# Optimization experiments

Measured on AMD Instinct MI355X. Metric: run time of the kernel, lower is better.

Reference implementation:

```python
import jax, jax.numpy as jnp
import numpy as np

N_ELEMENTS = 64  # StructureElementLayer(n_elements=64)


def setup_inputs() -> dict:
    key = jax.random.key(0)
    k1, k2 = jax.random.split(key)
    # x: [N, C, T, V] skeleton sequence (batch, coord channels, time, joints)
    x = jax.random.normal(k1, (256, 3, 256, 25), dtype=jnp.float32)
    # StructureElementLayer parameters (torch.rand init / ones*3 init)
    centres = jax.random.uniform(k2, (N_ELEMENTS, 2), dtype=jnp.float32)
    sharpness = jnp.ones((N_ELEMENTS, 2), dtype=jnp.float32) * 3.0
    return {"x": x, "centres": centres, "sharpness": sharpness}


def _mst_deaths(D):
    """Dim-0 Vietoris-Rips persistence deaths == MST edge weights (Prim's algorithm).

    D: [n, n] symmetric distance matrix. Returns [n-1] finite death values
    (births are all 0; the single essential (0, inf) pair contributes
    exp(-inf)=0 to the structure-element layer and is dropped).
    """
    n = D.shape[0]
    in_tree = jnp.zeros((n,), dtype=bool).at[0].set(True)
    dist = D[0]  # min distance from each node to the current tree

    def step(carry, _):
        in_tree, dist = carry
        d = jnp.where(in_tree, jnp.inf, dist)
        j = jnp.argmin(d)
        w = d[j]
        in_tree = in_tree.at[j].set(True)
        dist = jnp.minimum(dist, D[j])
        return (in_tree, dist), w

    (_, _), deaths = jax.lax.scan(step, (in_tree, dist), None, length=n - 1)
    return deaths


def _forward(x, centres, sharpness):
    xm = x.mean(1)                                  # [N, T, V]
    diff = xm[..., :, None] - xm[..., None, :]      # [N, T, V, V] pairwise joint diffs
    diff = diff.mean(-3)                            # [N, V, V]
    feat = jnp.linalg.norm(diff, axis=1)            # [N, V]  (torch.norm(., 2, dim=1))
    feat = (feat - feat.min()) / (feat.max() - feat.min())
    # Euclidean distance matrix of the N points in V-dim space (grad-safe sqrt)
    sq = jnp.sum(feat * feat, axis=1)
    D2 = sq[:, None] + sq[None, :] - 2.0 * (feat @ feat.T)
    D2 = jnp.maximum(D2, 0.0)
    D = jnp.where(D2 > 0.0, jnp.sqrt(jnp.where(D2 > 0.0, D2, 1.0)), 0.0)
    deaths = _mst_deaths(D)                         # [N-1]
    diag = jnp.stack([jnp.zeros_like(deaths), deaths], axis=-1)  # [N-1, 2] (birth, death)
    # StructureElementLayer: sum_i exp(-sum_d (p_id - c_kd)^2 * s_kd^2)
    d2 = (diag[:, None, :] - centres[None, :, :]) ** 2            # [N-1, K, 2]
    out = jnp.exp(-(d2 * (sharpness ** 2)).sum(-1)).sum(0)        # [K]
    return out


def reference(x, centres, sharpness):
    return _forward(x, centres, sharpness)
```

## Files before the change

### kernel.cpp

```cpp
#include <hip/hip_runtime.h>
#include <hip/hip_fp16.h>


#define WS_M    0
#define WS_MM   25600
#define WS_D16  65536

__global__ void k_mean(const float* __restrict__ x, float* __restrict__ m) {
    const int n = blockIdx.x;
    const int tid = threadIdx.x;
    __shared__ float sums[25];
    if (tid < 25) sums[tid] = 0.0f;
    __syncthreads();
    if (tid < 200) {
        const float* base = x + (long)n * 19200 + 4 * tid;
        float a0 = 0.f, a1 = 0.f, a2 = 0.f, a3 = 0.f;
        #pragma unroll
        for (int i = 0; i < 24; ++i) {
            float4 v = *reinterpret_cast<const float4*>(base + 800 * i);
            a0 += v.x; a1 += v.y; a2 += v.z; a3 += v.w;
        }
        const int v0 = (4 * tid) % 25;
        atomicAdd(&sums[v0], a0);
        atomicAdd(&sums[(v0 + 1) % 25], a1);
        atomicAdd(&sums[(v0 + 2) % 25], a2);
        atomicAdd(&sums[(v0 + 3) % 25], a3);
    }
    __syncthreads();
    if (tid < 25) m[n * 25 + tid] = sums[tid] * (1.0f / 768.0f);
}

__global__ void __launch_bounds__(256) k_dist(const float* __restrict__ m,
                                              unsigned short* __restrict__ D16,
                                              unsigned int* __restrict__ mm) {
    __shared__ float mS[6400];
    __shared__ float featS[6400];
    __shared__ unsigned int bmin, bmax;
    const int i = blockIdx.x;
    const int t = threadIdx.x;
    if (t == 0) { bmin = 0x7F800000u; bmax = 0u; }
    #pragma unroll
    for (int it = 0; it < 7; ++it) {
        int o = it * 256 + t;
        if (o < 1600) reinterpret_cast<float4*>(mS)[o] =
            reinterpret_cast<const float4*>(m)[o];
    }
    __syncthreads();
    float r[25];
    #pragma unroll
    for (int v = 0; v < 25; ++v) r[v] = mS[t * 25 + v];
    float S1 = 0.f, S2 = 0.f;
    #pragma unroll
    for (int v = 0; v < 25; ++v) { S1 += r[v]; S2 += r[v] * r[v]; }
    float fmn = 1e30f, fmx = -1e30f;
    #pragma unroll
    for (int w = 0; w < 25; ++w) {
        float q = S2 - 2.f * r[w] * S1 + 25.f * r[w] * r[w];
        q = fmaxf(q, 0.f);
        float f = sqrtf(q);
        featS[t * 25 + w] = f;
        fmn = fminf(fmn, f); fmx = fmaxf(fmx, f);
    }
    if (i == 0) {
        atomicMin(&bmin, __float_as_uint(fmn));
        atomicMax(&bmax, __float_as_uint(fmx));
    }
    __syncthreads();
    if (i == 0 && t == 0) { mm[0] = bmin; mm[1] = bmax; }
    float fi[25];
    #pragma unroll
    for (int v = 0; v < 25; ++v) fi[v] = featS[i * 25 + v];
    float s = 0.f;
    #pragma unroll
    for (int v = 0; v < 25; ++v) { float d = fi[v] - featS[t * 25 + v]; s += d * d; }
    D16[i * 256 + t] = __half_as_ushort(__float2half(s));
}

#define DSTR 264

__global__ void __launch_bounds__(1024) k_mst(const unsigned short* __restrict__ D16g,
                                              const unsigned int* __restrict__ mm,
                                              const float* __restrict__ centres,
                                              const float* __restrict__ sharp,
                                              float* __restrict__ out) {
    __shared__ __align__(16) unsigned short Dl[256 * DSTR];
    __shared__ __align__(8) unsigned char compA[256];
    __shared__ unsigned char parent[256];
    __shared__ unsigned int rowKey[256];
    __shared__ unsigned int compKey[256];
    __shared__ float deaths[256];
    __shared__ unsigned int dcount;
    __shared__ float outpart[1024];
    const int tid = threadIdx.x;

    {
        const uint4* src = reinterpret_cast<const uint4*>(D16g);
        #pragma unroll
        for (int it = 0; it < 8; ++it) {
            const int flat = it * 1024 + tid;
            const int rr = flat >> 5, cc = flat & 31;
            *reinterpret_cast<uint4*>(reinterpret_cast<char*>(Dl) + rr * (DSTR * 2) + cc * 16)
                = src[flat];
        }
    }
    if (tid < 256) compA[tid] = (unsigned char)tid;
    if (tid == 0) dcount = 0;
    __syncthreads();

    const int r = tid & 255;
    const int q = tid >> 8;
    const int jb0 = q * 64;
    const uint4* rowq = reinterpret_cast<const uint4*>(
        reinterpret_cast<const char*>(Dl) + r * (DSTR * 2) + jb0 * 2);
    const uint2* compv = reinterpret_cast<const uint2*>(compA);

    unsigned int cano[32];
    #pragma unroll
    for (int t2 = 0; t2 < 32; ++t2) {
        const int j0 = jb0 + 2 * t2, j1 = j0 + 1;
        const unsigned int c0 = (r < j0) ? (((unsigned)r << 8) | j0) : (((unsigned)j0 << 8) | r);
        const unsigned int c1 = (r < j1) ? (((unsigned)r << 8) | j1) : (((unsigned)j1 << 8) | r);
        cano[t2] = c0 | (c1 << 16);
    }

    int nc = 256;
    while (nc > 1) {
        if (tid < 256) { rowKey[tid] = 0xFFFFFFFFu; compKey[tid] = 0xFFFFFFFFu; }
        __syncthreads();

        const unsigned int myComp = compA[r];
        unsigned int best = 0xFFFFFFFFu;
        #pragma unroll
        for (int c8 = 0; c8 < 8; ++c8) {
            const uint4 w4 = rowq[c8];
            const uint2 c2 = compv[q * 8 + c8];
            const unsigned int wds[4] = {w4.x, w4.y, w4.z, w4.w};
            const unsigned int cbs[2] = {c2.x, c2.y};
            #pragma unroll
            for (int p = 0; p < 4; ++p) {
                const unsigned int ww = wds[p];
                const unsigned int cp = cano[c8 * 4 + p];
                unsigned int k0 = (ww << 16) | (cp & 0xFFFFu);
                unsigned int k1 = (ww & 0xFFFF0000u) | (cp >> 16);
                const unsigned int cj0 = (cbs[p >> 1] >> (16 * (p & 1))) & 0xFFu;
                const unsigned int cj1 = (cbs[p >> 1] >> (16 * (p & 1) + 8)) & 0xFFu;
                k0 = (cj0 != myComp) ? k0 : 0xFFFFFFFFu;
                k1 = (cj1 != myComp) ? k1 : 0xFFFFFFFFu;
                best = best < k0 ? best : k0;
                best = best < k1 ? best : k1;
            }
        }
        if (best != 0xFFFFFFFFu) atomicMin(&rowKey[r], best);
        __syncthreads();
        if (tid < 256) {
            const unsigned int rk = rowKey[tid];
            if (rk != 0xFFFFFFFFu) atomicMin(&compKey[compA[tid]], rk);
        }
        __syncthreads();

        unsigned int pk = 0xFFFFFFFFu;
        bool isRoot = false;
        unsigned int par = (unsigned int)tid;
        if (tid < 256) {
            pk = compKey[tid];
            isRoot = (compA[tid] == (unsigned char)tid);
            if (isRoot && pk != 0xFFFFFFFFu) {
                const unsigned int canon = pk & 0xFFFFu;
                const unsigned int u = canon >> 8, v = canon & 0xFFu;
                const unsigned int cu = compA[u], cv = compA[v];
                par = (cu == (unsigned int)tid) ? cv : cu;
            }
            parent[tid] = (unsigned char)par;
        }
        __syncthreads();

        if (tid < 256 && isRoot && par != (unsigned int)tid) {
            if (parent[par] == (unsigned char)tid && (unsigned int)tid < par) {
                parent[tid] = (unsigned char)tid;
            } else {
                const unsigned int di = atomicAdd(&dcount, 1u);
                deaths[di] = sqrtf(__half2float(__ushort_as_half((unsigned short)(pk >> 16))));
            }
        }
        __syncthreads();

        for (;;) {
            unsigned char p0 = 0, np = 0;
            if (tid < 256) { p0 = parent[tid]; np = parent[p0]; }
            const int cnt = __syncthreads_count(tid < 256 && np != p0);
            if (tid < 256) parent[tid] = np;
            __syncthreads();
            if (cnt == 0) break;
        }

        if (tid < 256) compA[tid] = parent[compA[tid]];
        nc = __syncthreads_count(tid < 256 && compA[tid] == (unsigned char)tid);
    }

    const float mn = __uint_as_float(mm[0]);
    const float mx = __uint_as_float(mm[1]);
    const float inv = 1.0f / (mx - mn);
    const int k = tid & 63;
    const int part = tid >> 6;
    const float c0 = centres[2 * k], c1 = centres[2 * k + 1];
    const float s0 = sharp[2 * k],   s1 = sharp[2 * k + 1];
    const float t0 = c0 * c0 * s0 * s0;
    const float s1sq = s1 * s1;
    float acc = 0.f;
    for (int idx = part; idx < 255; idx += 16) {
        const float d = deaths[idx] * inv - c1;
        acc += __expf(-(t0 + d * d * s1sq));
    }
    outpart[tid] = acc;
    __syncthreads();
    if (tid < 64) {
        float s = 0.f;
        #pragma unroll
        for (int pp = 0; pp < 16; ++pp) s += outpart[tid + 64 * pp];
        out[tid] = s;
    }
}

extern "C" void kernel_launch(void* const* d_in, const int* in_sizes, int n_in,
                              void* d_out, int out_size, void* d_ws, size_t ws_size,
                              hipStream_t stream) {
    const float* x       = (const float*)d_in[0];
    const float* centres = (const float*)d_in[1];
    const float* sharp   = (const float*)d_in[2];
    float* out = (float*)d_out;
    char* ws = (char*)d_ws;
    float*          m   = (float*)(ws + WS_M);
    unsigned int*   mm  = (unsigned int*)(ws + WS_MM);
    unsigned short* D16 = (unsigned short*)(ws + WS_D16);

    k_mean<<<256, 256, 0, stream>>>(x, m);
    k_dist<<<256, 256, 0, stream>>>(m, D16, mm);
    k_mst<<<1, 1024, 0, stream>>>(D16, mm, centres, sharp, out);
}
```

Before: 98.26 us.

## Contract Boruvka components into shrinking supernode distance matrices with fused first round

Computes each row's minimum edge key in the distance kernel via DPP wave reductions, so the first Boruvka round needs no full matrix scan in the MST kernel. After each round the components are relabeled densely and the distance matrix is contracted into a smaller component-to-component min matrix, ping-ponging between two shared buffers. Union/pointer-jumping work runs on a single wave with ballot instead of block-wide barriers. This cuts per-round scan work and barrier count, at the cost of many shared-memory atomicMin operations during contraction.

```diff
diff --git a/kernel.cpp b/kernel.cpp
--- a/kernel.cpp
+++ b/kernel.cpp
@@ -4,7 +4,10 @@
 
 #define WS_M    0
 #define WS_MM   25600
+#define WS_RK   28672
 #define WS_D16  65536
+
+#define INF32 0xFFFFFFFFu
 
 __global__ void k_mean(const float* __restrict__ x, float* __restrict__ m) {
     const int n = blockIdx.x;
@@ -30,12 +33,21 @@
     if (tid < 25) m[n * 25 + tid] = sums[tid] * (1.0f / 768.0f);
 }
 
+template <int CTRL>
+__device__ __forceinline__ unsigned int dpp_min_step(unsigned int v) {
+    unsigned int t = (unsigned int)__builtin_amdgcn_update_dpp(
+        (int)0xFFFFFFFF, (int)v, CTRL, 0xF, 0xF, false);
+    return (t < v) ? t : v;
+}
+
 __global__ void __launch_bounds__(256) k_dist(const float* __restrict__ m,
                                               unsigned short* __restrict__ D16,
+                                              unsigned int* __restrict__ rowKeyG,
                                               unsigned int* __restrict__ mm) {
     __shared__ float mS[6400];
     __shared__ float featS[6400];
     __shared__ unsigned int bmin, bmax;
+    __shared__ unsigned int wred[4];
     const int i = blockIdx.x;
     const int t = threadIdx.x;
     if (t == 0) { bmin = 0x7F800000u; bmax = 0u; }
@@ -73,128 +85,182 @@
     float s = 0.f;
     #pragma unroll
     for (int v = 0; v < 25; ++v) { float d = fi[v] - featS[t * 25 + v]; s += d * d; }
-    D16[i * 256 + t] = __half_as_ushort(__float2half(s));
-}
-
-#define DSTR 264
+    const unsigned int w16 = (unsigned int)__half_as_ushort(__float2half(s));
+    D16[i * 256 + t] = (unsigned short)w16;
+    const unsigned int lo = (i < t) ? i : t, hi = (i < t) ? t : i;
+    unsigned int key = (t == i) ? INF32 : ((w16 << 16) | (lo << 8) | hi);
+    key = dpp_min_step<0x111>(key);
+    key = dpp_min_step<0x112>(key);
+    key = dpp_min_step<0x114>(key);
+    key = dpp_min_step<0x118>(key);
+    key = dpp_min_step<0x142>(key);
+    key = dpp_min_step<0x143>(key);
+    if ((t & 63) == 63) wred[t >> 6] = key;
+    __syncthreads();
+    if (t == 0) {
+        unsigned int b0 = wred[0] < wred[1] ? wred[0] : wred[1];
+        unsigned int b1 = wred[2] < wred[3] ? wred[2] : wred[3];
+        rowKeyG[i] = b0 < b1 ? b0 : b1;
+    }
+}
+
+#define SA 132
+#define SB 68
+#define OFF_B (128 * SA)
+
+__device__ __forceinline__ void wave0_phase(int n, int lane,
+        unsigned int* rowKeyS, unsigned char* parentS, unsigned char* newidS,
+        unsigned char* cmapS, float* deaths, unsigned int* ncS, unsigned int* dcS) {
+    unsigned int par[4];
+    #pragma unroll
+    for (int s = 0; s < 4; ++s) {
+        const int i = lane + 64 * s;
+        if (i < n) {
+            const unsigned int rk = rowKeyS[i];
+            const unsigned int u = (rk >> 8) & 0xFFu, v = rk & 0xFFu;
+            unsigned int p = (u == (unsigned int)i) ? v : u;
+            if (rk == INF32) p = (unsigned int)i;
+            par[s] = p;
+            parentS[i] = (unsigned char)p;
+        }
+    }
+    #pragma unroll
+    for (int s = 0; s < 4; ++s) {
+        const int i = lane + 64 * s;
+        if (i < n) {
+            const unsigned int p = par[s];
+            if (p != (unsigned int)i) {
+                const unsigned int mp = parentS[p];
+                if (mp == (unsigned int)i && (unsigned int)i < p) {
+                    parentS[i] = (unsigned char)i;
+                } else {
+                    const unsigned int d = atomicAdd(dcS, 1u);
+                    const unsigned int rk = rowKeyS[i];
+                    deaths[d] = sqrtf(__half2float(__ushort_as_half(
+                        (unsigned short)(rk >> 16))));
+                }
+            }
+        }
+    }
+    for (;;) {
+        bool ch = false;
+        #pragma unroll
+        for (int s = 0; s < 4; ++s) {
+            const int i = lane + 64 * s;
+            if (i < n) {
+                const unsigned char p0 = parentS[i];
+                const unsigned char np = parentS[p0];
+                if (np != p0) { ch = true; parentS[i] = np; }
+            }
+        }
+        if (__ballot(ch) == 0ull) break;
+    }
+    #pragma unroll
+    for (int s = 0; s < 4; ++s) {
+        const int i = lane + 64 * s;
+        if (i < n && parentS[i] == (unsigned char)i)
+            newidS[i] = (unsigned char)atomicAdd(ncS, 1u);
+    }
+    #pragma unroll
+    for (int s = 0; s < 4; ++s) {
+        const int i = lane + 64 * s;
+        if (i < n) cmapS[i] = newidS[parentS[i]];
+    }
+}
 
 __global__ void __launch_bounds__(1024) k_mst(const unsigned short* __restrict__ D16g,
+                                              const unsigned int* __restrict__ rowKeyG,
                                               const unsigned int* __restrict__ mm,
                                               const float* __restrict__ centres,
                                               const float* __restrict__ sharp,
                                               float* __restrict__ out) {
-    __shared__ __align__(16) unsigned short Dl[256 * DSTR];
-    __shared__ __align__(8) unsigned char compA[256];
-    __shared__ unsigned char parent[256];
-    __shared__ unsigned int rowKey[256];
-    __shared__ unsigned int compKey[256];
+    __shared__ unsigned int Mb[128 * SA + 64 * SB];
+    __shared__ unsigned int rowKeyS[256];
+    __shared__ unsigned char parentS[256], newidS[256];
+    __shared__ __align__(8) unsigned char cmapS[256];
+    __shared__ unsigned int ncS, dcS;
     __shared__ float deaths[256];
-    __shared__ unsigned int dcount;
     __shared__ float outpart[1024];
     const int tid = threadIdx.x;
 
-    {
-        const uint4* src = reinterpret_cast<const uint4*>(D16g);
-        #pragma unroll
-        for (int it = 0; it < 8; ++it) {
-            const int flat = it * 1024 + tid;
-            const int rr = flat >> 5, cc = flat & 31;
-            *reinterpret_cast<uint4*>(reinterpret_cast<char*>(Dl) + rr * (DSTR * 2) + cc * 16)
-                = src[flat];
-        }
-    }
-    if (tid < 256) compA[tid] = (unsigned char)tid;
-    if (tid == 0) dcount = 0;
-    __syncthreads();
-
-    const int r = tid & 255;
-    const int q = tid >> 8;
-    const int jb0 = q * 64;
-    const uint4* rowq = reinterpret_cast<const uint4*>(
-        reinterpret_cast<const char*>(Dl) + r * (DSTR * 2) + jb0 * 2);
-    const uint2* compv = reinterpret_cast<const uint2*>(compA);
-
-    unsigned int cano[32];
-    #pragma unroll
-    for (int t2 = 0; t2 < 32; ++t2) {
-        const int j0 = jb0 + 2 * t2, j1 = j0 + 1;
-        const unsigned int c0 = (r < j0) ? (((unsigned)r << 8) | j0) : (((unsigned)j0 << 8) | r);
-        const unsigned int c1 = (r < j1) ? (((unsigned)r << 8) | j1) : (((unsigned)j1 << 8) | r);
-        cano[t2] = c0 | (c1 << 16);
-    }
-
-    int nc = 256;
-    while (nc > 1) {
-        if (tid < 256) { rowKey[tid] = 0xFFFFFFFFu; compKey[tid] = 0xFFFFFFFFu; }
-        __syncthreads();
-
-        const unsigned int myComp = compA[r];
-        unsigned int best = 0xFFFFFFFFu;
+    if (tid < 256) rowKeyS[tid] = rowKeyG[tid];
+    if (tid == 0) { ncS = 0; dcS = 0; }
+    __syncthreads();
+    if (tid < 64)
+        wave0_phase(256, tid, rowKeyS, parentS, newidS, cmapS, deaths, &ncS, &dcS);
+    __syncthreads();
+    int n = (int)ncS;
+
+    if (n > 1) {
+        for (int w = tid; w < n * SA; w += 1024) Mb[w] = INF32;
+        __syncthreads();
+        const int r = tid & 255, q = tid >> 8, jb0 = q * 64;
+        const unsigned int cr = cmapS[r];
+        const uint4* src = reinterpret_cast<const uint4*>(D16g) + r * 32 + q * 8;
+        const uint2* cmv = reinterpret_cast<const uint2*>(cmapS);
         #pragma unroll
         for (int c8 = 0; c8 < 8; ++c8) {
-            const uint4 w4 = rowq[c8];
-            const uint2 c2 = compv[q * 8 + c8];
+            const uint4 w4 = src[c8];
+            const uint2 c2 = cmv[q * 8 + c8];
             const unsigned int wds[4] = {w4.x, w4.y, w4.z, w4.w};
             const unsigned int cbs[2] = {c2.x, c2.y};
             #pragma unroll
-            for (int p = 0; p < 4; ++p) {
-                const unsigned int ww = wds[p];
-                const unsigned int cp = cano[c8 * 4 + p];
-                unsigned int k0 = (ww << 16) | (cp & 0xFFFFu);
-                unsigned int k1 = (ww & 0xFFFF0000u) | (cp >> 16);
-                const unsigned int cj0 = (cbs[p >> 1] >> (16 * (p & 1))) & 0xFFu;
-                const unsigned int cj1 = (cbs[p >> 1] >> (16 * (p & 1) + 8)) & 0xFFu;
-                k0 = (cj0 != myComp) ? k0 : 0xFFFFFFFFu;
-                k1 = (cj1 != myComp) ? k1 : 0xFFFFFFFFu;
-                best = best < k0 ? best : k0;
-                best = best < k1 ? best : k1;
-            }
-        }
-        if (best != 0xFFFFFFFFu) atomicMin(&rowKey[r], best);
-        __syncthreads();
-        if (tid < 256) {
-            const unsigned int rk = rowKey[tid];
-            if (rk != 0xFFFFFFFFu) atomicMin(&compKey[compA[tid]], rk);
-        }
-        __syncthreads();
-
-        unsigned int pk = 0xFFFFFFFFu;
-        bool isRoot = false;
-        unsigned int par = (unsigned int)tid;
-        if (tid < 256) {
-            pk = compKey[tid];
-            isRoot = (compA[tid] == (unsigned char)tid);
-            if (isRoot && pk != 0xFFFFFFFFu) {
-                const unsigned int canon = pk & 0xFFFFu;
-                const unsigned int u = canon >> 8, v = canon & 0xFFu;
-                const unsigned int cu = compA[u], cv = compA[v];
-                par = (cu == (unsigned int)tid) ? cv : cu;
-            }
-            parent[tid] = (unsigned char)par;
-        }
-        __syncthreads();
-
-        if (tid < 256 && isRoot && par != (unsigned int)tid) {
-            if (parent[par] == (unsigned char)tid && (unsigned int)tid < par) {
-                parent[tid] = (unsigned char)tid;
-            } else {
-                const unsigned int di = atomicAdd(&dcount, 1u);
-                deaths[di] = sqrtf(__half2float(__ushort_as_half((unsigned short)(pk >> 16))));
-            }
-        }
-        __syncthreads();
-
-        for (;;) {
-            unsigned char p0 = 0, np = 0;
-            if (tid < 256) { p0 = parent[tid]; np = parent[p0]; }
-            const int cnt = __syncthreads_count(tid < 256 && np != p0);
-            if (tid < 256) parent[tid] = np;
+            for (int u = 0; u < 8; ++u) {
+                const unsigned int cj = (cbs[u >> 2] >> (8 * (u & 3))) & 0xFFu;
+                if (cj != cr) {
+                    const unsigned int w16 = (wds[u >> 1] >> (16 * (u & 1))) & 0xFFFFu;
+                    const unsigned int lo = cr < cj ? cr : cj;
+                    const unsigned int hi = cr < cj ? cj : cr;
+                    atomicMin(&Mb[cr * SA + cj], (w16 << 16) | (lo << 8) | hi);
+                }
+            }
+        }
+        __syncthreads();
+    }
+
+    int srcOff = 0, srcStr = SA, dstOff = OFF_B, dstStr = SB;
+    while (n > 1) {
+        if (tid < n) rowKeyS[tid] = INF32;
+        if (tid == 0) ncS = 0;
+        __syncthreads();
+        if (tid < 8 * n) {
+            const int a = tid >> 3, sub = tid & 7;
+            const unsigned int* row = &Mb[srcOff + a * srcStr];
+            unsigned int best = INF32;
+            for (int b = sub; b < n; b += 8) {
+                const unsigned int v = row[b];
+                best = v < best ? v : best;
+            }
+            if (best != INF32) atomicMin(&rowKeyS[a], best);
+        }
+        __syncthreads();
+        if (tid < 64)
+            wave0_phase(n, tid, rowKeyS, parentS, newidS, cmapS, deaths, &ncS, &dcS);
+        __syncthreads();
+        const int nc = (int)ncS;
+        if (nc > 1) {
+            for (int w = tid; w < nc * dstStr; w += 1024) Mb[dstOff + w] = INF32;
             __syncthreads();
-            if (cnt == 0) break;
-        }
-
-        if (tid < 256) compA[tid] = parent[compA[tid]];
-        nc = __syncthreads_count(tid < 256 && compA[tid] == (unsigned char)tid);
+            if (tid < 8 * n) {
+                const int a = tid >> 3, sub = tid & 7;
+                const unsigned int ca = cmapS[a];
+                const unsigned int* row = &Mb[srcOff + a * srcStr];
+                for (int b = sub; b < n; b += 8) {
+                    const unsigned int cb = cmapS[b];
+                    const unsigned int v = row[b];
+                    if (ca != cb && v != INF32) {
+                        const unsigned int lo = ca < cb ? ca : cb;
+                        const unsigned int hi = ca < cb ? cb : ca;
+                        atomicMin(&Mb[dstOff + ca * dstStr + cb],
+                                  (v & 0xFFFF0000u) | (lo << 8) | hi);
+                    }
+                }
+            }
+            __syncthreads();
+        }
+        const int t1 = srcOff; srcOff = dstOff; dstOff = t1;
+        const int t2 = srcStr; srcStr = dstStr; dstStr = t2;
+        n = nc;
     }
 
     const float mn = __uint_as_float(mm[0]);
@@ -231,9 +297,10 @@
     char* ws = (char*)d_ws;
     float*          m   = (float*)(ws + WS_M);
     unsigned int*   mm  = (unsigned int*)(ws + WS_MM);
+    unsigned int*   rk  = (unsigned int*)(ws + WS_RK);
     unsigned short* D16 = (unsigned short*)(ws + WS_D16);
 
     k_mean<<<256, 256, 0, stream>>>(x, m);
-    k_dist<<<256, 256, 0, stream>>>(m, D16, mm);
-    k_mst<<<1, 1024, 0, stream>>>(D16, mm, centres, sharp, out);
-}
+    k_dist<<<256, 256, 0, stream>>>(m, D16, rk, mm);
+    k_mst<<<1, 1024, 0, stream>>>(D16, rk, mm, centres, sharp, out);
+}
```

Result: faster. 96.03 us (-2.3%).
